# Kernel tuning notes

Hardware: AMD Instinct MI355X
Metric: run time of the kernel (lower is better)

## Reference

```python
import jax, jax.numpy as jnp
import numpy as np

N_NODES = 100000
N_EDGES = 3200000
IN_F = 256
OUT_F = 128


def setup_inputs() -> dict:
    key = jax.random.key(0)
    k1, k2, k3, k4, k5, k6 = jax.random.split(key, 6)
    x = jax.random.normal(k1, (N_NODES, IN_F), dtype=jnp.float32)
    adj_rows = jax.random.randint(k2, (N_EDGES,), 0, N_NODES, dtype=jnp.int32)
    adj_cols = jax.random.randint(k3, (N_EDGES,), 0, N_NODES, dtype=jnp.int32)
    adj_vals = jax.random.uniform(k4, (N_EDGES,), dtype=jnp.float32)
    stdv = 1.0 / np.sqrt(IN_F)
    W = jax.random.uniform(k5, (IN_F, OUT_F), minval=-stdv, maxval=stdv, dtype=jnp.float32)
    b = jax.random.uniform(k6, (OUT_F,), minval=-stdv, maxval=stdv, dtype=jnp.float32)
    return {"x": x, "adj_rows": adj_rows, "adj_cols": adj_cols,
            "adj_vals": adj_vals, "W": W, "b": b}


def reference(x, adj_rows, adj_cols, adj_vals, W, b):
    # support = Linear(x): [N, out]
    support = x @ W + b
    # spmm(adj, support): out[i] = sum_{e: rows[e]==i} vals[e] * support[cols[e]]
    msgs = adj_vals[:, None] * support[adj_cols]  # [E, out]
    out = jax.ops.segment_sum(msgs, adj_rows, num_segments=N_NODES)
    return out
```

## Files before the change

kernel.cpp:

```cpp
#include <hip/hip_runtime.h>
#include <stdint.h>

#define NN 100000
#define NE 3200000
#define KF 256
#define MF 128

#define RB 64
#define NB ((NN + RB - 1) / RB)
#define EPB 8192
#define EPT (EPB / 256)
#define PGRID ((NE + EPB - 1) / EPB)
#define SCAPB 2560
#define RPT 10

typedef __attribute__((ext_vector_type(8))) short bf16x8;
typedef __attribute__((ext_vector_type(4))) float floatx4;

__device__ __forceinline__ unsigned short f2bf(float f) {
  union { float f; unsigned int i; } w; w.f = f;
  unsigned int u = w.i;
  u += 0x7FFFu + ((u >> 16) & 1u);
  return (unsigned short)(u >> 16);
}

__global__ __launch_bounds__(256) void wt_kernel(const float* __restrict__ W,
                                                 unsigned short* __restrict__ Wt,
                                                 unsigned int* __restrict__ cursor) {
  int idx = blockIdx.x * 256 + threadIdx.x;
  int k = idx >> 7;
  int c = idx & 127;
  Wt[(size_t)c * KF + k] = f2bf(W[(size_t)k * MF + c]);
  if (idx < NB) cursor[idx] = (unsigned int)idx * SCAPB;
}

__global__ __launch_bounds__(256) void gemm_kernel(const float* __restrict__ x,
                                                   const unsigned short* __restrict__ Wt,
                                                   const float* __restrict__ bias,
                                                   unsigned short* __restrict__ support) {
  __shared__ unsigned short Ax[64][72];
  __shared__ unsigned short Wl[128][72];
  const int tid = threadIdx.x;
  const int row0 = blockIdx.x * 64;
  const int lane = tid & 63;
  const int wv = tid >> 6;
  const int m = lane & 15;
  const int quad = lane >> 4;

  floatx4 acc[8];
#pragma unroll
  for (int t = 0; t < 8; ++t) acc[t] = (floatx4){0.f, 0.f, 0.f, 0.f};

  for (int kb = 0; kb < 4; ++kb) {
    if (kb) __syncthreads();
#pragma unroll
    for (int i = 0; i < 4; ++i) {
      int u = tid + i * 256;
      int r = u >> 4;
      int q = u & 15;
      float4 v = make_float4(0.f, 0.f, 0.f, 0.f);
      if (row0 + r < NN)
        v = *(const float4*)(x + (size_t)(row0 + r) * KF + kb * 64 + q * 4);
      ushort4 p;
      p.x = f2bf(v.x); p.y = f2bf(v.y); p.z = f2bf(v.z); p.w = f2bf(v.w);
      *(ushort4*)(&Ax[r][q * 4]) = p;
    }
#pragma unroll
    for (int i = 0; i < 4; ++i) {
      int u = tid + i * 256;
      int c = u >> 3;
      int kq = u & 7;
      *(uint4*)(&Wl[c][kq * 8]) = *(const uint4*)(Wt + (size_t)c * KF + kb * 64 + kq * 8);
    }
    __syncthreads();
#pragma unroll
    for (int kc = 0; kc < 2; ++kc) {
      int k0 = kc * 32 + quad * 8;
      bf16x8 af = *(const bf16x8*)(&Ax[wv * 16 + m][k0]);
#pragma unroll
      for (int ct = 0; ct < 8; ++ct) {
        bf16x8 bfv = *(const bf16x8*)(&Wl[ct * 16 + m][k0]);
        acc[ct] = __builtin_amdgcn_mfma_f32_16x16x32_bf16(af, bfv, acc[ct], 0, 0, 0);
      }
    }
  }
#pragma unroll
  for (int ct = 0; ct < 8; ++ct) {
    int col = ct * 16 + m;
    float bv = bias[col];
#pragma unroll
    for (int rg = 0; rg < 4; ++rg) {
      int grow = row0 + wv * 16 + quad * 4 + rg;
      if (grow < NN)
        support[(size_t)grow * MF + col] = f2bf(acc[ct][rg] + bv);
    }
  }
}

__global__ __launch_bounds__(256) void part_kernel(const int* __restrict__ rows,
                                                   const int* __restrict__ cols,
                                                   const float* __restrict__ vals,
                                                   unsigned int* __restrict__ cursor,
                                                   uint2* __restrict__ binned) {
  __shared__ unsigned int hist[NB];
  __shared__ unsigned int base[NB];
  const int tid = threadIdx.x;
  const int e0 = blockIdx.x * EPB;
  for (int i = tid; i < NB; i += 256) hist[i] = 0u;
  __syncthreads();
  unsigned int pk[EPT];
#pragma unroll
  for (int k = 0; k < EPT; ++k) {
    int e = e0 + tid + k * 256;
    if (e < NE) {
      unsigned int r = (unsigned int)rows[e];
      unsigned int rank = atomicAdd(&hist[r >> 6], 1u);
      pk[k] = r | (rank << 17);
    } else pk[k] = 0xFFFFFFFFu;
  }
  __syncthreads();
  for (int i = tid; i < NB; i += 256) {
    unsigned int c = hist[i];
    base[i] = c ? atomicAdd(&cursor[i], c) : 0u;
  }
  __syncthreads();
#pragma unroll
  for (int k = 0; k < EPT; ++k) {
    if (pk[k] != 0xFFFFFFFFu) {
      int e = e0 + tid + k * 256;
      unsigned int r = pk[k] & 0x1FFFFu;
      unsigned int rank = pk[k] >> 17;
      unsigned int b = r >> 6;
      unsigned int pos = base[b] + rank;
      if (pos < (b + 1u) * SCAPB) {
        unsigned int key = ((r & 63u) << 17) | (unsigned int)cols[e];
        binned[pos] = make_uint2(key, __float_as_uint(vals[e]));
      }
    }
  }
}

#define FMA4(ev, sv) { \
    float v_ = __uint_as_float((ev).y); \
    a0 = fmaf(v_, __uint_as_float((sv).x << 16), a0); \
    a1 = fmaf(v_, __uint_as_float((sv).x & 0xFFFF0000u), a1); \
    a2 = fmaf(v_, __uint_as_float((sv).y << 16), a2); \
    a3 = fmaf(v_, __uint_as_float((sv).y & 0xFFFF0000u), a3); \
  }

__global__ __launch_bounds__(256) void sortgather_kernel(const unsigned int* __restrict__ cursor,
                                                         const uint2* __restrict__ binned,
                                                         const unsigned int* __restrict__ support_u,
                                                         float* __restrict__ out) {
  __shared__ uint2 stage[SCAPB];
  __shared__ unsigned int lcnt[RB];
  __shared__ unsigned int lbase[RB + 1];
  const int tid = threadIdx.x;
  const unsigned int start = blockIdx.x * SCAPB;
  unsigned int end = cursor[blockIdx.x];
  if (end > start + SCAPB) end = start + SCAPB;
  if (tid < RB) lcnt[tid] = 0u;
  __syncthreads();
  uint2 rec[RPT];
  unsigned short rk[RPT];
  unsigned short rl_[RPT];
#pragma unroll
  for (int k = 0; k < RPT; ++k) {
    unsigned int i = start + (unsigned int)tid + (unsigned int)k * 256u;
    rec[k] = make_uint2(0u, 0u); rk[k] = 0; rl_[k] = 0xFFFFu;
    if (i < end) {
      rec[k] = binned[i];
      unsigned int rl = rec[k].x >> 17;
      rl_[k] = (unsigned short)rl;
      rk[k] = (unsigned short)atomicAdd(&lcnt[rl], 1u);
    }
  }
  __syncthreads();
  if (tid < 64) {
    unsigned int v = lcnt[tid];
    unsigned int inc = v;
#pragma unroll
    for (int d = 1; d < 64; d <<= 1) {
      unsigned int n = __shfl_up(inc, d, 64);
      if (tid >= d) inc += n;
    }
    lbase[tid] = inc - v;
    if (tid == 63) lbase[64] = inc;
  }
  __syncthreads();
#pragma unroll
  for (int k = 0; k < RPT; ++k) {
    if (rl_[k] != 0xFFFFu) {
      unsigned int pos = lbase[rl_[k]] + (unsigned int)rk[k];
      if (pos < SCAPB) stage[pos] = make_uint2(rec[k].x & 0x1FFFFu, rec[k].y);
    }
  }
  __syncthreads();
  const int lane = tid & 63;
  const int wv = tid >> 6;
  const int half = lane >> 5;
  const int hl = lane & 31;
  const int node0 = blockIdx.x * RB;
#pragma unroll 1
  for (int nn = 0; nn < 16; ++nn) {
    const int rl = wv * 16 + nn;
    const int node = node0 + rl;
    unsigned int i = lbase[rl];
    const unsigned int e = lbase[rl + 1];
    float a0 = 0.f, a1 = 0.f, a2 = 0.f, a3 = 0.f;
    for (; i + 8 <= e; i += 8) {
      unsigned int j = i + half * 4;
      uint2 e0 = stage[j + 0];
      uint2 e1 = stage[j + 1];
      uint2 e2 = stage[j + 2];
      uint2 e3 = stage[j + 3];
      uint2 s0 = *(const uint2*)(support_u + (size_t)e0.x * 64 + hl * 2);
      uint2 s1 = *(const uint2*)(support_u + (size_t)e1.x * 64 + hl * 2);
      uint2 s2 = *(const uint2*)(support_u + (size_t)e2.x * 64 + hl * 2);
      uint2 s3 = *(const uint2*)(support_u + (size_t)e3.x * 64 + hl * 2);
      FMA4(e0, s0); FMA4(e1, s1); FMA4(e2, s2); FMA4(e3, s3);
    }
    if (i + 4 <= e) {
      unsigned int j = i + half * 2;
      uint2 e0 = stage[j + 0];
      uint2 e1 = stage[j + 1];
      uint2 s0 = *(const uint2*)(support_u + (size_t)e0.x * 64 + hl * 2);
      uint2 s1 = *(const uint2*)(support_u + (size_t)e1.x * 64 + hl * 2);
      FMA4(e0, s0); FMA4(e1, s1);
      i += 4;
    }
    if (i + 2 <= e) {
      uint2 e0 = stage[i + half];
      uint2 s0 = *(const uint2*)(support_u + (size_t)e0.x * 64 + hl * 2);
      FMA4(e0, s0);
      i += 2;
    }
    if (i < e && half == 0) {
      uint2 e0 = stage[i];
      uint2 s0 = *(const uint2*)(support_u + (size_t)e0.x * 64 + hl * 2);
      FMA4(e0, s0);
    }
    a0 += __shfl(a0, hl + 32);
    a1 += __shfl(a1, hl + 32);
    a2 += __shfl(a2, hl + 32);
    a3 += __shfl(a3, hl + 32);
    if (half == 0 && node < NN) {
      float4 o = make_float4(a0, a1, a2, a3);
      *(float4*)(out + (size_t)node * MF + hl * 4) = o;
    }
  }
}

extern "C" void kernel_launch(void* const* d_in, const int* in_sizes, int n_in,
                              void* d_out, int out_size, void* d_ws, size_t ws_size,
                              hipStream_t stream) {
  const float* x    = (const float*)d_in[0];
  const int*   rows = (const int*)d_in[1];
  const int*   cols = (const int*)d_in[2];
  const float* vals = (const float*)d_in[3];
  const float* W    = (const float*)d_in[4];
  const float* bias = (const float*)d_in[5];

  char* ws = (char*)d_ws;
  unsigned short* Wt      = (unsigned short*)ws;
  unsigned short* support = (unsigned short*)(ws + 65536);
  uint2*          binned  = (uint2*)(ws + 65536 + 25600000ull);
  unsigned int*   cursor  = (unsigned int*)(ws + 57675776ull);

  wt_kernel<<<128, 256, 0, stream>>>(W, Wt, cursor);
  gemm_kernel<<<(NN + 63) / 64, 256, 0, stream>>>(x, Wt, bias, support);
  part_kernel<<<PGRID, 256, 0, stream>>>(rows, cols, vals, cursor, binned);
  sortgather_kernel<<<NB, 256, 0, stream>>>(cursor, binned,
                                            (const unsigned int*)support, (float*)d_out);
}
```

Before: 419.1 us.

## Split GEMM waves by column tiles and widen partition blocks to 1024 threads

The GEMM now gives each wave two 16-column tiles across all 64 rows instead of one 16-row strip across all 128 columns. Each wave therefore loads all four A fragments and only two W fragments per k-step, which changes the LDS read pattern and reuse. Separately, the partition kernel runs 1024 threads per block with 8 edges per thread instead of 256 threads with 32 edges per thread. This spreads the histogram clear and cursor reservation loops across more threads and raises parallelism per block, at the cost of higher per-block resource use.

```diff
diff --git a/kernel.cpp b/kernel.cpp
--- a/kernel.cpp
+++ b/kernel.cpp
@@ -9,7 +9,8 @@
 #define RB 64
 #define NB ((NN + RB - 1) / RB)
 #define EPB 8192
-#define EPT (EPB / 256)
+#define PTH 1024
+#define EPT (EPB / PTH)
 #define PGRID ((NE + EPB - 1) / EPB)
 #define SCAPB 2560
 #define RPT 10
@@ -47,9 +48,11 @@
   const int m = lane & 15;
   const int quad = lane >> 4;
 
-  floatx4 acc[8];
-#pragma unroll
-  for (int t = 0; t < 8; ++t) acc[t] = (floatx4){0.f, 0.f, 0.f, 0.f};
+  floatx4 acc[4][2];
+#pragma unroll
+  for (int rt = 0; rt < 4; ++rt)
+#pragma unroll
+    for (int c2 = 0; c2 < 2; ++c2) acc[rt][c2] = (floatx4){0.f, 0.f, 0.f, 0.f};
 
   for (int kb = 0; kb < 4; ++kb) {
     if (kb) __syncthreads();
@@ -76,28 +79,36 @@
 #pragma unroll
     for (int kc = 0; kc < 2; ++kc) {
       int k0 = kc * 32 + quad * 8;
-      bf16x8 af = *(const bf16x8*)(&Ax[wv * 16 + m][k0]);
-#pragma unroll
-      for (int ct = 0; ct < 8; ++ct) {
-        bf16x8 bfv = *(const bf16x8*)(&Wl[ct * 16 + m][k0]);
-        acc[ct] = __builtin_amdgcn_mfma_f32_16x16x32_bf16(af, bfv, acc[ct], 0, 0, 0);
+      bf16x8 af[4];
+#pragma unroll
+      for (int rt = 0; rt < 4; ++rt)
+        af[rt] = *(const bf16x8*)(&Ax[rt * 16 + m][k0]);
+#pragma unroll
+      for (int c2 = 0; c2 < 2; ++c2) {
+        bf16x8 bfv = *(const bf16x8*)(&Wl[(wv * 2 + c2) * 16 + m][k0]);
+#pragma unroll
+        for (int rt = 0; rt < 4; ++rt)
+          acc[rt][c2] = __builtin_amdgcn_mfma_f32_16x16x32_bf16(af[rt], bfv, acc[rt][c2], 0, 0, 0);
       }
     }
   }
 #pragma unroll
-  for (int ct = 0; ct < 8; ++ct) {
-    int col = ct * 16 + m;
+  for (int c2 = 0; c2 < 2; ++c2) {
+    int col = (wv * 2 + c2) * 16 + m;
     float bv = bias[col];
 #pragma unroll
-    for (int rg = 0; rg < 4; ++rg) {
-      int grow = row0 + wv * 16 + quad * 4 + rg;
-      if (grow < NN)
-        support[(size_t)grow * MF + col] = f2bf(acc[ct][rg] + bv);
-    }
-  }
-}
-
-__global__ __launch_bounds__(256) void part_kernel(const int* __restrict__ rows,
+    for (int rt = 0; rt < 4; ++rt) {
+#pragma unroll
+      for (int rg = 0; rg < 4; ++rg) {
+        int grow = row0 + rt * 16 + quad * 4 + rg;
+        if (grow < NN)
+          support[(size_t)grow * MF + col] = f2bf(acc[rt][c2][rg] + bv);
+      }
+    }
+  }
+}
+
+__global__ __launch_bounds__(PTH) void part_kernel(const int* __restrict__ rows,
                                                    const int* __restrict__ cols,
                                                    const float* __restrict__ vals,
                                                    unsigned int* __restrict__ cursor,
@@ -106,12 +117,12 @@
   __shared__ unsigned int base[NB];
   const int tid = threadIdx.x;
   const int e0 = blockIdx.x * EPB;
-  for (int i = tid; i < NB; i += 256) hist[i] = 0u;
+  for (int i = tid; i < NB; i += PTH) hist[i] = 0u;
   __syncthreads();
   unsigned int pk[EPT];
 #pragma unroll
   for (int k = 0; k < EPT; ++k) {
-    int e = e0 + tid + k * 256;
+    int e = e0 + tid + k * PTH;
     if (e < NE) {
       unsigned int r = (unsigned int)rows[e];
       unsigned int rank = atomicAdd(&hist[r >> 6], 1u);
@@ -119,7 +130,7 @@
     } else pk[k] = 0xFFFFFFFFu;
   }
   __syncthreads();
-  for (int i = tid; i < NB; i += 256) {
+  for (int i = tid; i < NB; i += PTH) {
     unsigned int c = hist[i];
     base[i] = c ? atomicAdd(&cursor[i], c) : 0u;
   }
@@ -127,7 +138,7 @@
 #pragma unroll
   for (int k = 0; k < EPT; ++k) {
     if (pk[k] != 0xFFFFFFFFu) {
-      int e = e0 + tid + k * 256;
+      int e = e0 + tid + k * PTH;
       unsigned int r = pk[k] & 0x1FFFFu;
       unsigned int rank = pk[k] >> 17;
       unsigned int b = r >> 6;
@@ -269,7 +280,7 @@
 
   wt_kernel<<<128, 256, 0, stream>>>(W, Wt, cursor);
   gemm_kernel<<<(NN + 63) / 64, 256, 0, stream>>>(x, Wt, bias, support);
-  part_kernel<<<PGRID, 256, 0, stream>>>(rows, cols, vals, cursor, binned);
+  part_kernel<<<PGRID, PTH, 0, stream>>>(rows, cols, vals, cursor, binned);
   sortgather_kernel<<<NB, 256, 0, stream>>>(cursor, binned,
                                             (const unsigned int*)support, (float*)d_out);
 }
```

After: 399.5 us. 4.7% less time.
